# Kernel tuning notes

Measured on AMD Instinct MI355X. Metric: run time of the kernel, lower is better.

Reference implementation:

```python
import jax, jax.numpy as jnp
import numpy as np

B, C, D, H, W = 4, 128, 16, 16, 16
HID = 128
EPS = 1e-5


def setup_inputs() -> dict:
    key = jax.random.key(0)
    ks = jax.random.split(key, 10)
    s = 1.0 / np.sqrt(C)
    return {
        "x": jax.random.normal(ks[0], (B, C, D, H, W), dtype=jnp.float32),
        "Wq": jax.random.normal(ks[1], (HID, C), dtype=jnp.float32) * s,
        "bq": jax.random.normal(ks[2], (HID,), dtype=jnp.float32) * s,
        "Wk": jax.random.normal(ks[3], (HID, C), dtype=jnp.float32) * s,
        "bk": jax.random.normal(ks[4], (HID,), dtype=jnp.float32) * s,
        "Wv": jax.random.normal(ks[5], (HID, C), dtype=jnp.float32) * s,
        "bv": jax.random.normal(ks[6], (HID,), dtype=jnp.float32) * s,
        "bn_weight": jax.random.normal(ks[7], (HID,), dtype=jnp.float32),
        "bn_bias": jax.random.normal(ks[8], (HID,), dtype=jnp.float32),
        "gamma": jax.random.normal(ks[9], (1,), dtype=jnp.float32),
    }


def reference(x, Wq, bq, Wk, bk, Wv, bv, bn_weight, bn_bias, gamma):
    b, c, d, h, w = x.shape
    n = d * h * w
    xf = x.reshape(b, c, n)  # [B, C, N]
    # 1x1 conv3d == per-voxel linear: [B, hid, N]
    q = jnp.einsum("hc,bcn->bnh", Wq, xf) + bq  # [B, N, hid] (query permuted)
    k = jnp.einsum("hc,bcn->bhn", Wk, xf) + bk[None, :, None]  # [B, hid, N]
    v = jnp.einsum("hc,bcn->bhn", Wv, xf) + bv[None, :, None]  # [B, hid, N]
    # unscaled attention scores [B, N, N], softmax over last dim
    attn = jax.nn.softmax(jnp.einsum("bih,bhj->bij", q, k), axis=-1)
    # out[b,h,i] = sum_j v[b,h,j] * attn[b,i,j]
    out = jnp.einsum("bhj,bij->bhi", v, attn)  # [B, hid, N]
    # BatchNorm3d (training mode): per-channel stats over (B, N), biased var
    mean = jnp.mean(out, axis=(0, 2), keepdims=True)
    var = jnp.mean(jnp.square(out - mean), axis=(0, 2), keepdims=True)
    out = (out - mean) * jax.lax.rsqrt(var + EPS)
    out = out * bn_weight[None, :, None] + bn_bias[None, :, None]
    out = gamma[0] * out.reshape(b, c, d, h, w) + x
    return out
```

## Files before the change

kernel.cpp:

```cpp
#include <hip/hip_runtime.h>


#define NV 4096
#define LOG2E 1.44269504088896340736f
#define EPSV 1e-5f

typedef float f32x4 __attribute__((ext_vector_type(4)));
typedef short bf16x8 __attribute__((ext_vector_type(8)));
typedef unsigned short u16x4 __attribute__((ext_vector_type(4)));
typedef unsigned int u32x2 __attribute__((ext_vector_type(2)));

static __device__ __forceinline__ unsigned short f2bf(float f) {
    union { float f; unsigned u; } v; v.f = f;
    unsigned r = v.u + 0x7FFFu + ((v.u >> 16) & 1u);
    return (unsigned short)(r >> 16);
}
static __device__ __forceinline__ float bf2f(unsigned short u) {
    union { unsigned u; float f; } v; v.u = ((unsigned)u) << 16; return v.f;
}
static __device__ __forceinline__ unsigned fbits(float f) {
    union { float f; unsigned u; } v; v.f = f; return v.u;
}

__global__ __launch_bounds__(256) void convw_kernel(
    const float* __restrict__ Wq, const float* __restrict__ Wk,
    const float* __restrict__ Wv, unsigned short* __restrict__ Wbf)
{
    int i = blockIdx.x * 256 + threadIdx.x;
    const float* src = (i < 16384) ? Wq : (i < 32768 ? Wk : Wv);
    Wbf[i] = f2bf(src[i & 16383]);
}

__global__ __launch_bounds__(256) void xt_kernel(
    const float* __restrict__ x, unsigned short* __restrict__ xT)
{
    __shared__ unsigned short st[64 * 132];
    const int b = blockIdx.x >> 6, n0 = (blockIdx.x & 63) << 6;
    const int t = threadIdx.x;
    #pragma unroll
    for (int it = 0; it < 32; ++it) {
        const int e = it * 256 + t;
        const int c = e >> 6, il = e & 63;
        st[il * 132 + c] = f2bf(x[(((b << 7) + c) << 12) + n0 + il]);
    }
    __syncthreads();
    unsigned short* dst = xT + (((b << 12) + n0) << 7);
    #pragma unroll
    for (int it = 0; it < 32; ++it) {
        const int e = it * 256 + t;
        const int il = e >> 7, c = e & 127;
        dst[(il << 7) + c] = st[il * 132 + c];
    }
}

__global__ __launch_bounds__(256) void proj_kernel(
    const unsigned short* __restrict__ xT,
    const unsigned short* __restrict__ Wbf,
    const float* __restrict__ bq, const float* __restrict__ bk,
    const float* __restrict__ bv,
    unsigned short* __restrict__ Qb, unsigned short* __restrict__ Kb,
    unsigned short* __restrict__ Vb)
{
    __shared__ unsigned short vtile[128 * 66];
    const int bid = blockIdx.x;
    const int m = bid >> 8, b = (bid >> 6) & 3, n0 = (bid & 63) << 6;
    const int t = threadIdx.x, w = t >> 6, lane = t & 63;
    const int quad = lane >> 4, l16 = lane & 15;
    const int vb = n0 + (w << 4);

    bf16x8 af[4];
    {
        const unsigned short* xr = xT + (((b << 12) + vb + l16) << 7) + (quad << 3);
        #pragma unroll
        for (int ck = 0; ck < 4; ++ck) af[ck] = *(const bf16x8*)(xr + (ck << 5));
    }
    const unsigned short* Wm = Wbf + (m << 14);
    const float* bias = (m == 0) ? bq : ((m == 1) ? bk : bv);
    unsigned short* dst = (m == 0) ? Qb : Kb;

    #pragma unroll
    for (int s = 0; s < 8; ++s) {
        const int h = (s << 4) + l16;
        f32x4 acc = {0.f, 0.f, 0.f, 0.f};
        #pragma unroll
        for (int ck = 0; ck < 4; ++ck) {
            bf16x8 wf = *(const bf16x8*)(Wm + (h << 7) + (ck << 5) + (quad << 3));
            acc = __builtin_amdgcn_mfma_f32_16x16x32_bf16(af[ck], wf, acc, 0, 0, 0);
        }
        const float bval = bias[h];
        if (m == 2) {
            #pragma unroll
            for (int r = 0; r < 4; ++r)
                vtile[h * 66 + (w << 4) + (quad << 2) + r] = f2bf(acc[r] + bval);
        } else {
            #pragma unroll
            for (int r = 0; r < 4; ++r) {
                const int n = vb + (quad << 2) + r;
                dst[(((b << 12) + n) << 7) + h] = f2bf(acc[r] + bval);
            }
        }
    }
    if (m == 2) {
        __syncthreads();
        #pragma unroll
        for (int it = 0; it < 32; ++it) {
            const int e = it * 256 + t;
            const int h = e >> 6, il = e & 63;
            Vb[(((b << 7) + h) << 12) + n0 + il] = vtile[h * 66 + il];
        }
    }
}

template<int NSL>
__global__ __launch_bounds__(256, 2) void flash_kernel(
    const unsigned short* __restrict__ Qb,
    const unsigned short* __restrict__ Kb,
    const unsigned short* __restrict__ Vb,
    unsigned short* __restrict__ Opart, float* __restrict__ lpart,
    unsigned short* __restrict__ Obuf)
{
    __shared__ unsigned short Kt[64 * 128];
    __shared__ unsigned short Vt[128 * 64];
    __shared__ unsigned short pA[4][32 * 72];
    const int bid = blockIdx.x;
    const int sl = bid >> 7, b = (bid >> 5) & 3, ic = bid & 31;
    const int t = threadIdx.x, w = t >> 6, lane = t & 63;
    const int quad = lane >> 4, l16 = lane & 15;
    const int iw = (ic << 7) + (w << 5);
    const int jbase = sl * (NV / NSL);
    unsigned short* pAw = pA[w];

    const int ktg = t & 15, ktj = t >> 4;
    const int vtg = t & 7,  vth = t >> 3;
    const int kswz = (ktg ^ ktj) << 3;
    const int vswz = (vtg ^ (vth & 7)) << 3;

    bf16x8 qf[2][4];
    #pragma unroll
    for (int half = 0; half < 2; ++half) {
        const unsigned short* qp =
            Qb + (((b << 12) + iw + (half << 4) + l16) << 7) + (quad << 3);
        #pragma unroll
        for (int ck = 0; ck < 4; ++ck) qf[half][ck] = *(const bf16x8*)(qp + (ck << 5));
    }
    f32x4 Oacc[2][8];
    #pragma unroll
    for (int half = 0; half < 2; ++half)
        #pragma unroll
        for (int s = 0; s < 8; ++s) Oacc[half][s] = (f32x4){0.f, 0.f, 0.f, 0.f};
    float lsum0 = 0.f, lsum1 = 0.f;

    const unsigned short* Kbb = Kb + ((long)b << 19);
    const unsigned short* Vbb = Vb + ((long)b << 19);

    for (int t8 = 0; t8 < (NV / NSL) >> 6; ++t8) {
        const int j0 = jbase + (t8 << 6);

        __syncthreads();
        bf16x8 sk[4], sv[4];
        #pragma unroll
        for (int r = 0; r < 4; ++r)
            sk[r] = *(const bf16x8*)(Kbb + ((j0 + (r << 4) + ktj) << 7) + (ktg << 3));
        #pragma unroll
        for (int r = 0; r < 4; ++r)
            sv[r] = *(const bf16x8*)(Vbb + (((r << 5) + vth) << 12) + j0 + (vtg << 3));
        #pragma unroll
        for (int r = 0; r < 4; ++r)
            *(bf16x8*)(Kt + (((r << 4) + ktj) << 7) + kswz) = sk[r];
        #pragma unroll
        for (int r = 0; r < 4; ++r)
            *(bf16x8*)(Vt + (((r << 5) + vth) << 6) + vswz) = sv[r];
        __syncthreads();

        #pragma unroll
        for (int js = 0; js < 4; ++js) {
            bf16x8 kf[4];
            const int krow = ((js << 4) + l16) << 7;
            #pragma unroll
            for (int ck = 0; ck < 4; ++ck)
                kf[ck] = *(const bf16x8*)(Kt + krow + ((((ck << 2) + quad) ^ l16) << 3));
            f32x4 a0 = {0.f, 0.f, 0.f, 0.f}, a1 = {0.f, 0.f, 0.f, 0.f};
            #pragma unroll
            for (int ck = 0; ck < 4; ++ck) {
                a0 = __builtin_amdgcn_mfma_f32_16x16x32_bf16(kf[ck], qf[0][ck], a0, 0, 0, 0);
                a1 = __builtin_amdgcn_mfma_f32_16x16x32_bf16(kf[ck], qf[1][ck], a1, 0, 0, 0);
            }
            f32x4 e0, e1;
            #pragma unroll
            for (int r = 0; r < 4; ++r) {
                e0[r] = exp2f(a0[r] * LOG2E);
                e1[r] = exp2f(a1[r] * LOG2E);
            }
            lsum0 += (e0[0] + e0[1]) + (e0[2] + e0[3]);
            lsum1 += (e1[0] + e1[1]) + (e1[2] + e1[3]);
            u32x2 pk0, pk1;
            pk0[0] = __builtin_amdgcn_perm(fbits(e0[1]), fbits(e0[0]), 0x07060302u);
            pk0[1] = __builtin_amdgcn_perm(fbits(e0[3]), fbits(e0[2]), 0x07060302u);
            pk1[0] = __builtin_amdgcn_perm(fbits(e1[1]), fbits(e1[0]), 0x07060302u);
            pk1[1] = __builtin_amdgcn_perm(fbits(e1[3]), fbits(e1[2]), 0x07060302u);
            const int jc = (js << 4) + (quad << 2);
            *(u32x2*)(pAw + l16 * 72 + jc)        = pk0;
            *(u32x2*)(pAw + (16 + l16) * 72 + jc) = pk1;
        }
        bf16x8 pf[2][2];
        #pragma unroll
        for (int half = 0; half < 2; ++half)
            #pragma unroll
            for (int kh = 0; kh < 2; ++kh)
                pf[half][kh] = *(const bf16x8*)(pAw + ((half << 4) + l16) * 72 +
                                                (kh << 5) + (quad << 3));
        #pragma unroll
        for (int s = 0; s < 8; ++s) {
            const int vrow = ((s << 4) + l16) << 6;
            const bf16x8 v0 = *(const bf16x8*)(Vt + vrow + ((quad ^ (l16 & 7)) << 3));
            const bf16x8 v1 = *(const bf16x8*)(Vt + vrow + (((4 + quad) ^ (l16 & 7)) << 3));
            Oacc[0][s] = __builtin_amdgcn_mfma_f32_16x16x32_bf16(v0, pf[0][0], Oacc[0][s], 0, 0, 0);
            Oacc[0][s] = __builtin_amdgcn_mfma_f32_16x16x32_bf16(v1, pf[0][1], Oacc[0][s], 0, 0, 0);
            Oacc[1][s] = __builtin_amdgcn_mfma_f32_16x16x32_bf16(v0, pf[1][0], Oacc[1][s], 0, 0, 0);
            Oacc[1][s] = __builtin_amdgcn_mfma_f32_16x16x32_bf16(v1, pf[1][1], Oacc[1][s], 0, 0, 0);
        }
    }

    float l0 = lsum0; l0 += __shfl_xor(l0, 16); l0 += __shfl_xor(l0, 32);
    float l1 = lsum1; l1 += __shfl_xor(l1, 16); l1 += __shfl_xor(l1, 32);

    if (NSL == 1) {
        const float rl0 = 1.f / l0, rl1 = 1.f / l1;
        #pragma unroll
        for (int s = 0; s < 8; ++s)
            #pragma unroll
            for (int r = 0; r < 4; ++r) {
                const int h = (s << 4) + (quad << 2) + r;
                Obuf[(((b << 7) + h) << 12) + iw + l16]      = f2bf(Oacc[0][s][r] * rl0);
                Obuf[(((b << 7) + h) << 12) + iw + 16 + l16] = f2bf(Oacc[1][s][r] * rl1);
            }
    } else {
        const int slb = (sl << 2) + b;
        if (quad == 0) {
            lpart[(slb << 12) + iw + l16]      = l0;
            lpart[(slb << 12) + iw + 16 + l16] = l1;
        }
        unsigned short* Ob = Opart + ((long)slb << 19);
        #pragma unroll
        for (int half = 0; half < 2; ++half)
            #pragma unroll
            for (int s = 0; s < 8; ++s)
                #pragma unroll
                for (int r = 0; r < 4; ++r) {
                    const int h = (s << 4) + (quad << 2) + r;
                    Ob[(h << 12) + iw + (half << 4) + l16] = f2bf(Oacc[half][s][r]);
                }
    }
}

template<int NSL>
__global__ __launch_bounds__(256) void merge_kernel(
    const unsigned short* __restrict__ Opart, const float* __restrict__ lpart,
    unsigned short* __restrict__ Obuf, float* __restrict__ psums)
{
    const int bid = blockIdx.x;
    const int b = bid >> 9, h = (bid >> 2) & 127, iq = bid & 3;
    const int t = threadIdx.x;
    const int ibase = (iq << 10) + (t << 2);
    float a0 = 0.f, a1 = 0.f, a2 = 0.f, a3 = 0.f;
    float t0 = 0.f, t1 = 0.f, t2 = 0.f, t3 = 0.f;
    #pragma unroll
    for (int sl = 0; sl < NSL; ++sl) {
        const int slb = (sl << 2) + b;
        const u16x4 u  = *(const u16x4*)(Opart + ((long)slb << 19) + ((long)h << 12) + ibase);
        const float4 lv = *(const float4*)(lpart + (slb << 12) + ibase);
        a0 += bf2f(u[0]); a1 += bf2f(u[1]); a2 += bf2f(u[2]); a3 += bf2f(u[3]);
        t0 += lv.x; t1 += lv.y; t2 += lv.z; t3 += lv.w;
    }
    const float o0 = a0 / t0, o1 = a1 / t1, o2 = a2 / t2, o3 = a3 / t3;
    u16x4 o;
    o[0] = f2bf(o0); o[1] = f2bf(o1); o[2] = f2bf(o2); o[3] = f2bf(o3);
    *(u16x4*)(Obuf + (((b << 7) + h) << 12) + ibase) = o;

    float so  = o0 + o1 + o2 + o3;
    float so2 = o0*o0 + o1*o1 + o2*o2 + o3*o3;
    #pragma unroll
    for (int off = 32; off; off >>= 1) {
        so  += __shfl_down(so, off);
        so2 += __shfl_down(so2, off);
    }
    __shared__ float rb[8];
    const int wv = t >> 6;
    if ((t & 63) == 0) { rb[wv] = so; rb[4 + wv] = so2; }
    __syncthreads();
    if (t == 0) {
        psums[bid]        = rb[0] + rb[1] + rb[2] + rb[3];
        psums[2048 + bid] = rb[4] + rb[5] + rb[6] + rb[7];
    }
}

__global__ __launch_bounds__(256) void bnsum_kernel(
    const unsigned short* __restrict__ Obuf, float* __restrict__ psums)
{
    const int bid = blockIdx.x;
    const int b = bid >> 9, h = (bid >> 2) & 127, iq = bid & 3;
    const int t = threadIdx.x;
    const int ibase = (iq << 10) + (t << 2);
    const u16x4 u = *(const u16x4*)(Obuf + (((b << 7) + h) << 12) + ibase);
    const float x0 = bf2f(u[0]), x1 = bf2f(u[1]), x2 = bf2f(u[2]), x3 = bf2f(u[3]);
    float so  = x0 + x1 + x2 + x3;
    float so2 = x0*x0 + x1*x1 + x2*x2 + x3*x3;
    #pragma unroll
    for (int off = 32; off; off >>= 1) {
        so  += __shfl_down(so, off);
        so2 += __shfl_down(so2, off);
    }
    __shared__ float rb[8];
    const int wv = t >> 6;
    if ((t & 63) == 0) { rb[wv] = so; rb[4 + wv] = so2; }
    __syncthreads();
    if (t == 0) {
        psums[bid]        = rb[0] + rb[1] + rb[2] + rb[3];
        psums[2048 + bid] = rb[4] + rb[5] + rb[6] + rb[7];
    }
}

__global__ __launch_bounds__(256) void final_kernel(
    const unsigned short* __restrict__ Obuf, const float* __restrict__ x,
    const float* __restrict__ psums, const float* __restrict__ bnw,
    const float* __restrict__ bnb, const float* __restrict__ gammap,
    float* __restrict__ out)
{
    const int bid = blockIdx.x;
    const int c = (bid >> 2) & 127;
    const int t = threadIdx.x;
    const int li = t & 15;
    const int pid = ((li >> 2) << 9) + (c << 2) + (li & 3);
    float s  = psums[pid];
    float ss = psums[2048 + pid];
    s += __shfl_xor(s, 1, 16); ss += __shfl_xor(ss, 1, 16);
    s += __shfl_xor(s, 2, 16); ss += __shfl_xor(ss, 2, 16);
    s += __shfl_xor(s, 4, 16); ss += __shfl_xor(ss, 4, 16);
    s += __shfl_xor(s, 8, 16); ss += __shfl_xor(ss, 8, 16);
    const float inv = 1.f / 16384.f;
    const float mean = s * inv;
    const float var  = ss * inv - mean * mean;
    const float g = gammap[0];
    const float scale = bnw[c] * rsqrtf(var + EPSV);
    const float a  = g * scale;
    const float bb = g * (bnb[c] - mean * scale);

    const int base = (bid * 256 + t) << 2;
    const u16x4 u = *(const u16x4*)(Obuf + base);
    const float4 xv = *(const float4*)(x + base);
    float4 r;
    r.x = bf2f(u[0]) * a + bb + xv.x;
    r.y = bf2f(u[1]) * a + bb + xv.y;
    r.z = bf2f(u[2]) * a + bb + xv.z;
    r.w = bf2f(u[3]) * a + bb + xv.w;
    *(float4*)(out + base) = r;
}

extern "C" void kernel_launch(void* const* d_in, const int* in_sizes, int n_in,
                              void* d_out, int out_size, void* d_ws, size_t ws_size,
                              hipStream_t stream) {
    const float* x   = (const float*)d_in[0];
    const float* Wq  = (const float*)d_in[1];
    const float* bq  = (const float*)d_in[2];
    const float* Wk  = (const float*)d_in[3];
    const float* bk  = (const float*)d_in[4];
    const float* Wv  = (const float*)d_in[5];
    const float* bv  = (const float*)d_in[6];
    const float* bnw = (const float*)d_in[7];
    const float* bnb = (const float*)d_in[8];
    const float* gam = (const float*)d_in[9];
    float* out = (float*)d_out;

    char* ws = (char*)d_ws;
    unsigned short* xT   = (unsigned short*)(ws);
    unsigned short* Obuf = (unsigned short*)(ws);
    unsigned short* Qb   = (unsigned short*)(ws + (4u  << 20));
    unsigned short* Kb   = (unsigned short*)(ws + (8u  << 20));
    unsigned short* Vb   = (unsigned short*)(ws + (12u << 20));
    unsigned short* Wbf  = (unsigned short*)(ws + (16u << 20));
    float*          lpart = (float*)(ws + (16u << 20) + (128u << 10));
    float*          psums = (float*)(ws + (16u << 20) + (640u << 10));
    unsigned short* Opart = (unsigned short*)(ws + (17u << 20));

    int nsl = 1;
    if      (ws_size >= (17ull << 20) + (32ull << 20)) nsl = 8;
    else if (ws_size >= (17ull << 20) + (16ull << 20)) nsl = 4;
    else if (ws_size >= (17ull << 20) + (8ull  << 20)) nsl = 2;

    convw_kernel<<<192, 256, 0, stream>>>(Wq, Wk, Wv, Wbf);
    xt_kernel<<<256, 256, 0, stream>>>(x, xT);
    proj_kernel<<<768, 256, 0, stream>>>(xT, Wbf, bq, bk, bv, Qb, Kb, Vb);
    if (nsl == 8) {
        flash_kernel<8><<<1024, 256, 0, stream>>>(Qb, Kb, Vb, Opart, lpart, Obuf);
        merge_kernel<8><<<2048, 256, 0, stream>>>(Opart, lpart, Obuf, psums);
    } else if (nsl == 4) {
        flash_kernel<4><<<512, 256, 0, stream>>>(Qb, Kb, Vb, Opart, lpart, Obuf);
        merge_kernel<4><<<2048, 256, 0, stream>>>(Opart, lpart, Obuf, psums);
    } else if (nsl == 2) {
        flash_kernel<2><<<256, 256, 0, stream>>>(Qb, Kb, Vb, Opart, lpart, Obuf);
        merge_kernel<2><<<2048, 256, 0, stream>>>(Opart, lpart, Obuf, psums);
    } else {
        flash_kernel<1><<<128, 256, 0, stream>>>(Qb, Kb, Vb, Opart, lpart, Obuf);
        bnsum_kernel<<<2048, 256, 0, stream>>>(Obuf, psums);
    }
    final_kernel<<<2048, 256, 0, stream>>>(Obuf, x, psums, bnw, bnb, gam, out);
}
```

Measured before the change: 160.2 us.

## Fuse projection prep kernels and merge split-softmax with batchnorm finalize

```diff
diff --git a/kernel.cpp b/kernel.cpp
--- a/kernel.cpp
+++ b/kernel.cpp
@@ -8,6 +8,7 @@
 typedef float f32x4 __attribute__((ext_vector_type(4)));
 typedef short bf16x8 __attribute__((ext_vector_type(8)));
 typedef unsigned short u16x4 __attribute__((ext_vector_type(4)));
+typedef unsigned short u16x8 __attribute__((ext_vector_type(8)));
 typedef unsigned int u32x2 __attribute__((ext_vector_type(2)));
 
 static __device__ __forceinline__ unsigned short f2bf(float f) {
@@ -22,92 +23,86 @@
     union { float f; unsigned u; } v; v.f = f; return v.u;
 }
 
-__global__ __launch_bounds__(256) void convw_kernel(
+__global__ __launch_bounds__(256) void projx_kernel(
+    const float* __restrict__ x,
     const float* __restrict__ Wq, const float* __restrict__ Wk,
-    const float* __restrict__ Wv, unsigned short* __restrict__ Wbf)
-{
-    int i = blockIdx.x * 256 + threadIdx.x;
-    const float* src = (i < 16384) ? Wq : (i < 32768 ? Wk : Wv);
-    Wbf[i] = f2bf(src[i & 16383]);
-}
-
-__global__ __launch_bounds__(256) void xt_kernel(
-    const float* __restrict__ x, unsigned short* __restrict__ xT)
-{
-    __shared__ unsigned short st[64 * 132];
-    const int b = blockIdx.x >> 6, n0 = (blockIdx.x & 63) << 6;
-    const int t = threadIdx.x;
-    #pragma unroll
-    for (int it = 0; it < 32; ++it) {
-        const int e = it * 256 + t;
-        const int c = e >> 6, il = e & 63;
-        st[il * 132 + c] = f2bf(x[(((b << 7) + c) << 12) + n0 + il]);
-    }
-    __syncthreads();
-    unsigned short* dst = xT + (((b << 12) + n0) << 7);
-    #pragma unroll
-    for (int it = 0; it < 32; ++it) {
-        const int e = it * 256 + t;
-        const int il = e >> 7, c = e & 127;
-        dst[(il << 7) + c] = st[il * 132 + c];
-    }
-}
-
-__global__ __launch_bounds__(256) void proj_kernel(
-    const unsigned short* __restrict__ xT,
-    const unsigned short* __restrict__ Wbf,
+    const float* __restrict__ Wv,
     const float* __restrict__ bq, const float* __restrict__ bk,
     const float* __restrict__ bv,
     unsigned short* __restrict__ Qb, unsigned short* __restrict__ Kb,
     unsigned short* __restrict__ Vb)
 {
+    __shared__ unsigned short xt[64 * 136];
+    __shared__ unsigned short Wl[128 * 136];
     __shared__ unsigned short vtile[128 * 66];
-    const int bid = blockIdx.x;
-    const int m = bid >> 8, b = (bid >> 6) & 3, n0 = (bid & 63) << 6;
+    const int b = blockIdx.x >> 6, n0 = (blockIdx.x & 63) << 6;
     const int t = threadIdx.x, w = t >> 6, lane = t & 63;
     const int quad = lane >> 4, l16 = lane & 15;
-    const int vb = n0 + (w << 4);
+
+    #pragma unroll
+    for (int it = 0; it < 32; ++it) {
+        const int e = it * 256 + t;
+        const int c = e >> 6, il = e & 63;
+        xt[il * 136 + c] = f2bf(x[(((b << 7) + c) << 12) + n0 + il]);
+    }
+    __syncthreads();
 
     bf16x8 af[4];
     {
-        const unsigned short* xr = xT + (((b << 12) + vb + l16) << 7) + (quad << 3);
-        #pragma unroll
-        for (int ck = 0; ck < 4; ++ck) af[ck] = *(const bf16x8*)(xr + (ck << 5));
-    }
-    const unsigned short* Wm = Wbf + (m << 14);
-    const float* bias = (m == 0) ? bq : ((m == 1) ? bk : bv);
-    unsigned short* dst = (m == 0) ? Qb : Kb;
-
-    #pragma unroll
-    for (int s = 0; s < 8; ++s) {
-        const int h = (s << 4) + l16;
-        f32x4 acc = {0.f, 0.f, 0.f, 0.f};
-        #pragma unroll
-        for (int ck = 0; ck < 4; ++ck) {
-            bf16x8 wf = *(const bf16x8*)(Wm + (h << 7) + (ck << 5) + (quad << 3));
-            acc = __builtin_amdgcn_mfma_f32_16x16x32_bf16(af[ck], wf, acc, 0, 0, 0);
-        }
-        const float bval = bias[h];
-        if (m == 2) {
-            #pragma unroll
-            for (int r = 0; r < 4; ++r)
-                vtile[h * 66 + (w << 4) + (quad << 2) + r] = f2bf(acc[r] + bval);
-        } else {
-            #pragma unroll
-            for (int r = 0; r < 4; ++r) {
-                const int n = vb + (quad << 2) + r;
-                dst[(((b << 12) + n) << 7) + h] = f2bf(acc[r] + bval);
+        const int il = (w << 4) + l16;
+        #pragma unroll
+        for (int ck = 0; ck < 4; ++ck)
+            af[ck] = *(const bf16x8*)(xt + il * 136 + (ck << 5) + (quad << 3));
+    }
+    const int vb = n0 + (w << 4);
+    const float* Ws[3] = {Wq, Wk, Wv};
+    const float* bs[3] = {bq, bk, bv};
+
+    for (int m = 0; m < 3; ++m) {
+        __syncthreads();
+        #pragma unroll
+        for (int it = 0; it < 16; ++it) {
+            const int idx = it * 1024 + (t << 2);
+            const float4 wv4 = *(const float4*)(Ws[m] + idx);
+            const int h = idx >> 7, c = idx & 127;
+            u16x4 pk;
+            pk[0] = f2bf(wv4.x); pk[1] = f2bf(wv4.y);
+            pk[2] = f2bf(wv4.z); pk[3] = f2bf(wv4.w);
+            *(u16x4*)(Wl + h * 136 + c) = pk;
+        }
+        __syncthreads();
+
+        const float* bias = bs[m];
+        unsigned short* dst = (m == 0) ? Qb : Kb;
+        #pragma unroll
+        for (int s = 0; s < 8; ++s) {
+            const int h = (s << 4) + l16;
+            f32x4 acc = {0.f, 0.f, 0.f, 0.f};
+            #pragma unroll
+            for (int ck = 0; ck < 4; ++ck) {
+                const bf16x8 wf = *(const bf16x8*)(Wl + h * 136 + (ck << 5) + (quad << 3));
+                acc = __builtin_amdgcn_mfma_f32_16x16x32_bf16(af[ck], wf, acc, 0, 0, 0);
             }
-        }
-    }
-    if (m == 2) {
-        __syncthreads();
-        #pragma unroll
-        for (int it = 0; it < 32; ++it) {
-            const int e = it * 256 + t;
-            const int h = e >> 6, il = e & 63;
-            Vb[(((b << 7) + h) << 12) + n0 + il] = vtile[h * 66 + il];
-        }
+            const float bval = bias[h];
+            if (m == 2) {
+                #pragma unroll
+                for (int r = 0; r < 4; ++r)
+                    vtile[h * 66 + (w << 4) + (quad << 2) + r] = f2bf(acc[r] + bval);
+            } else {
+                #pragma unroll
+                for (int r = 0; r < 4; ++r) {
+                    const int n = vb + (quad << 2) + r;
+                    dst[(((b << 12) + n) << 7) + h] = f2bf(acc[r] + bval);
+                }
+            }
+        }
+    }
+    __syncthreads();
+    #pragma unroll
+    for (int it = 0; it < 32; ++it) {
+        const int e = it * 256 + t;
+        const int h = e >> 6, il = e & 63;
+        Vb[(((b << 7) + h) << 12) + n0 + il] = vtile[h * 66 + il];
     }
 }
 
@@ -155,7 +150,6 @@
 
     for (int t8 = 0; t8 < (NV / NSL) >> 6; ++t8) {
         const int j0 = jbase + (t8 << 6);
-
         __syncthreads();
         bf16x8 sk[4], sv[4];
         #pragma unroll
@@ -254,106 +248,131 @@
 }
 
 template<int NSL>
-__global__ __launch_bounds__(256) void merge_kernel(
+__global__ __launch_bounds__(1024) void mf_kernel(
     const unsigned short* __restrict__ Opart, const float* __restrict__ lpart,
-    unsigned short* __restrict__ Obuf, float* __restrict__ psums)
-{
-    const int bid = blockIdx.x;
-    const int b = bid >> 9, h = (bid >> 2) & 127, iq = bid & 3;
-    const int t = threadIdx.x;
-    const int ibase = (iq << 10) + (t << 2);
-    float a0 = 0.f, a1 = 0.f, a2 = 0.f, a3 = 0.f;
-    float t0 = 0.f, t1 = 0.f, t2 = 0.f, t3 = 0.f;
-    #pragma unroll
-    for (int sl = 0; sl < NSL; ++sl) {
-        const int slb = (sl << 2) + b;
-        const u16x4 u  = *(const u16x4*)(Opart + ((long)slb << 19) + ((long)h << 12) + ibase);
-        const float4 lv = *(const float4*)(lpart + (slb << 12) + ibase);
-        a0 += bf2f(u[0]); a1 += bf2f(u[1]); a2 += bf2f(u[2]); a3 += bf2f(u[3]);
-        t0 += lv.x; t1 += lv.y; t2 += lv.z; t3 += lv.w;
-    }
-    const float o0 = a0 / t0, o1 = a1 / t1, o2 = a2 / t2, o3 = a3 / t3;
-    u16x4 o;
-    o[0] = f2bf(o0); o[1] = f2bf(o1); o[2] = f2bf(o2); o[3] = f2bf(o3);
-    *(u16x4*)(Obuf + (((b << 7) + h) << 12) + ibase) = o;
-
-    float so  = o0 + o1 + o2 + o3;
-    float so2 = o0*o0 + o1*o1 + o2*o2 + o3*o3;
-    #pragma unroll
-    for (int off = 32; off; off >>= 1) {
-        so  += __shfl_down(so, off);
-        so2 += __shfl_down(so2, off);
-    }
-    __shared__ float rb[8];
-    const int wv = t >> 6;
-    if ((t & 63) == 0) { rb[wv] = so; rb[4 + wv] = so2; }
-    __syncthreads();
-    if (t == 0) {
-        psums[bid]        = rb[0] + rb[1] + rb[2] + rb[3];
-        psums[2048 + bid] = rb[4] + rb[5] + rb[6] + rb[7];
-    }
-}
-
-__global__ __launch_bounds__(256) void bnsum_kernel(
-    const unsigned short* __restrict__ Obuf, float* __restrict__ psums)
-{
-    const int bid = blockIdx.x;
-    const int b = bid >> 9, h = (bid >> 2) & 127, iq = bid & 3;
-    const int t = threadIdx.x;
-    const int ibase = (iq << 10) + (t << 2);
-    const u16x4 u = *(const u16x4*)(Obuf + (((b << 7) + h) << 12) + ibase);
-    const float x0 = bf2f(u[0]), x1 = bf2f(u[1]), x2 = bf2f(u[2]), x3 = bf2f(u[3]);
-    float so  = x0 + x1 + x2 + x3;
-    float so2 = x0*x0 + x1*x1 + x2*x2 + x3*x3;
-    #pragma unroll
-    for (int off = 32; off; off >>= 1) {
-        so  += __shfl_down(so, off);
-        so2 += __shfl_down(so2, off);
-    }
-    __shared__ float rb[8];
-    const int wv = t >> 6;
-    if ((t & 63) == 0) { rb[wv] = so; rb[4 + wv] = so2; }
-    __syncthreads();
-    if (t == 0) {
-        psums[bid]        = rb[0] + rb[1] + rb[2] + rb[3];
-        psums[2048 + bid] = rb[4] + rb[5] + rb[6] + rb[7];
-    }
-}
-
-__global__ __launch_bounds__(256) void final_kernel(
-    const unsigned short* __restrict__ Obuf, const float* __restrict__ x,
-    const float* __restrict__ psums, const float* __restrict__ bnw,
+    const float* __restrict__ x, const float* __restrict__ bnw,
     const float* __restrict__ bnb, const float* __restrict__ gammap,
     float* __restrict__ out)
 {
-    const int bid = blockIdx.x;
-    const int c = (bid >> 2) & 127;
+    const int h = blockIdx.x;
     const int t = threadIdx.x;
-    const int li = t & 15;
-    const int pid = ((li >> 2) << 9) + (c << 2) + (li & 3);
-    float s  = psums[pid];
-    float ss = psums[2048 + pid];
-    s += __shfl_xor(s, 1, 16); ss += __shfl_xor(ss, 1, 16);
-    s += __shfl_xor(s, 2, 16); ss += __shfl_xor(ss, 2, 16);
-    s += __shfl_xor(s, 4, 16); ss += __shfl_xor(ss, 4, 16);
-    s += __shfl_xor(s, 8, 16); ss += __shfl_xor(ss, 8, 16);
+    const int b = t >> 8;
+    const int i0 = (t & 255) << 4;
+
+    float A[16], L[16];
+    #pragma unroll
+    for (int k = 0; k < 16; ++k) { A[k] = 0.f; L[k] = 0.f; }
+    #pragma unroll
+    for (int sl = 0; sl < NSL; ++sl) {
+        const int slb = (sl << 2) + b;
+        const u16x8 u0 = *(const u16x8*)(Opart + ((long)slb << 19) + ((long)h << 12) + i0);
+        const u16x8 u1 = *(const u16x8*)(Opart + ((long)slb << 19) + ((long)h << 12) + i0 + 8);
+        const float* lp = lpart + (slb << 12) + i0;
+        #pragma unroll
+        for (int k = 0; k < 8; ++k) { A[k] += bf2f(u0[k]); A[8 + k] += bf2f(u1[k]); }
+        #pragma unroll
+        for (int k = 0; k < 4; ++k) {
+            const float4 lv = *(const float4*)(lp + (k << 2));
+            L[(k << 2) + 0] += lv.x; L[(k << 2) + 1] += lv.y;
+            L[(k << 2) + 2] += lv.z; L[(k << 2) + 3] += lv.w;
+        }
+    }
+    float o[16], s = 0.f, ss = 0.f;
+    #pragma unroll
+    for (int k = 0; k < 16; ++k) {
+        o[k] = A[k] / L[k];
+        s += o[k]; ss += o[k] * o[k];
+    }
+    #pragma unroll
+    for (int off = 32; off; off >>= 1) {
+        s  += __shfl_down(s, off);
+        ss += __shfl_down(ss, off);
+    }
+    __shared__ float rs[16], rss[16], fin[2];
+    const int wid = t >> 6;
+    if ((t & 63) == 0) { rs[wid] = s; rss[wid] = ss; }
+    __syncthreads();
+    if (t == 0) {
+        float s2 = 0.f, ss2 = 0.f;
+        #pragma unroll
+        for (int k = 0; k < 16; ++k) { s2 += rs[k]; ss2 += rss[k]; }
+        fin[0] = s2; fin[1] = ss2;
+    }
+    __syncthreads();
     const float inv = 1.f / 16384.f;
-    const float mean = s * inv;
-    const float var  = ss * inv - mean * mean;
+    const float mean = fin[0] * inv;
+    const float var  = fin[1] * inv - mean * mean;
     const float g = gammap[0];
-    const float scale = bnw[c] * rsqrtf(var + EPSV);
+    const float scale = bnw[h] * rsqrtf(var + EPSV);
     const float a  = g * scale;
-    const float bb = g * (bnb[c] - mean * scale);
-
-    const int base = (bid * 256 + t) << 2;
-    const u16x4 u = *(const u16x4*)(Obuf + base);
-    const float4 xv = *(const float4*)(x + base);
-    float4 r;
-    r.x = bf2f(u[0]) * a + bb + xv.x;
-    r.y = bf2f(u[1]) * a + bb + xv.y;
-    r.z = bf2f(u[2]) * a + bb + xv.z;
-    r.w = bf2f(u[3]) * a + bb + xv.w;
-    *(float4*)(out + base) = r;
+    const float bb = g * (bnb[h] - mean * scale);
+
+    const float* xp = x + (((b << 7) + h) << 12) + i0;
+    float* op = out + (((b << 7) + h) << 12) + i0;
+    #pragma unroll
+    for (int k = 0; k < 4; ++k) {
+        const float4 xv = *(const float4*)(xp + (k << 2));
+        float4 r;
+        r.x = o[(k << 2) + 0] * a + bb + xv.x;
+        r.y = o[(k << 2) + 1] * a + bb + xv.y;
+        r.z = o[(k << 2) + 2] * a + bb + xv.z;
+        r.w = o[(k << 2) + 3] * a + bb + xv.w;
+        *(float4*)(op + (k << 2)) = r;
+    }
+}
+
+__global__ __launch_bounds__(1024) void mf1_kernel(
+    const unsigned short* __restrict__ Obuf,
+    const float* __restrict__ x, const float* __restrict__ bnw,
+    const float* __restrict__ bnb, const float* __restrict__ gammap,
+    float* __restrict__ out)
+{
+    const int h = blockIdx.x;
+    const int t = threadIdx.x;
+    const int b = t >> 8;
+    const int i0 = (t & 255) << 4;
+    const u16x8 u0 = *(const u16x8*)(Obuf + (((b << 7) + h) << 12) + i0);
+    const u16x8 u1 = *(const u16x8*)(Obuf + (((b << 7) + h) << 12) + i0 + 8);
+    float o[16], s = 0.f, ss = 0.f;
+    #pragma unroll
+    for (int k = 0; k < 8; ++k) { o[k] = bf2f(u0[k]); o[8 + k] = bf2f(u1[k]); }
+    #pragma unroll
+    for (int k = 0; k < 16; ++k) { s += o[k]; ss += o[k] * o[k]; }
+    #pragma unroll
+    for (int off = 32; off; off >>= 1) {
+        s  += __shfl_down(s, off);
+        ss += __shfl_down(ss, off);
+    }
+    __shared__ float rs[16], rss[16], fin[2];
+    const int wid = t >> 6;
+    if ((t & 63) == 0) { rs[wid] = s; rss[wid] = ss; }
+    __syncthreads();
+    if (t == 0) {
+        float s2 = 0.f, ss2 = 0.f;
+        #pragma unroll
+        for (int k = 0; k < 16; ++k) { s2 += rs[k]; ss2 += rss[k]; }
+        fin[0] = s2; fin[1] = ss2;
+    }
+    __syncthreads();
+    const float inv = 1.f / 16384.f;
+    const float mean = fin[0] * inv;
+    const float var  = fin[1] * inv - mean * mean;
+    const float g = gammap[0];
+    const float scale = bnw[h] * rsqrtf(var + EPSV);
+    const float a  = g * scale;
+    const float bb = g * (bnb[h] - mean * scale);
+    const float* xp = x + (((b << 7) + h) << 12) + i0;
+    float* op = out + (((b << 7) + h) << 12) + i0;
+    #pragma unroll
+    for (int k = 0; k < 4; ++k) {
+        const float4 xv = *(const float4*)(xp + (k << 2));
+        float4 r;
+        r.x = o[(k << 2) + 0] * a + bb + xv.x;
+        r.y = o[(k << 2) + 1] * a + bb + xv.y;
+        r.z = o[(k << 2) + 2] * a + bb + xv.z;
+        r.w = o[(k << 2) + 3] * a + bb + xv.w;
+        *(float4*)(op + (k << 2)) = r;
+    }
 }
 
 extern "C" void kernel_launch(void* const* d_in, const int* in_sizes, int n_in,
@@ -372,14 +391,11 @@
     float* out = (float*)d_out;
 
     char* ws = (char*)d_ws;
-    unsigned short* xT   = (unsigned short*)(ws);
     unsigned short* Obuf = (unsigned short*)(ws);
     unsigned short* Qb   = (unsigned short*)(ws + (4u  << 20));
     unsigned short* Kb   = (unsigned short*)(ws + (8u  << 20));
     unsigned short* Vb   = (unsigned short*)(ws + (12u << 20));
-    unsigned short* Wbf  = (unsigned short*)(ws + (16u << 20));
     float*          lpart = (float*)(ws + (16u << 20) + (128u << 10));
-    float*          psums = (float*)(ws + (16u << 20) + (640u << 10));
     unsigned short* Opart = (unsigned short*)(ws + (17u << 20));
 
     int nsl = 1;
@@ -387,21 +403,18 @@
     else if (ws_size >= (17ull << 20) + (16ull << 20)) nsl = 4;
     else if (ws_size >= (17ull << 20) + (8ull  << 20)) nsl = 2;
 
-    convw_kernel<<<192, 256, 0, stream>>>(Wq, Wk, Wv, Wbf);
-    xt_kernel<<<256, 256, 0, stream>>>(x, xT);
-    proj_kernel<<<768, 256, 0, stream>>>(xT, Wbf, bq, bk, bv, Qb, Kb, Vb);
+    projx_kernel<<<256, 256, 0, stream>>>(x, Wq, Wk, Wv, bq, bk, bv, Qb, Kb, Vb);
     if (nsl == 8) {
         flash_kernel<8><<<1024, 256, 0, stream>>>(Qb, Kb, Vb, Opart, lpart, Obuf);
-        merge_kernel<8><<<2048, 256, 0, stream>>>(Opart, lpart, Obuf, psums);
+        mf_kernel<8><<<128, 1024, 0, stream>>>(Opart, lpart, x, bnw, bnb, gam, out);
     } else if (nsl == 4) {
         flash_kernel<4><<<512, 256, 0, stream>>>(Qb, Kb, Vb, Opart, lpart, Obuf);
-        merge_kernel<4><<<2048, 256, 0, stream>>>(Opart, lpart, Obuf, psums);
+        mf_kernel<4><<<128, 1024, 0, stream>>>(Opart, lpart, x, bnw, bnb, gam, out);
     } else if (nsl == 2) {
         flash_kernel<2><<<256, 256, 0, stream>>>(Qb, Kb, Vb, Opart, lpart, Obuf);
-        merge_kernel<2><<<2048, 256, 0, stream>>>(Opart, lpart, Obuf, psums);
+        mf_kernel<2><<<128, 1024, 0, stream>>>(Opart, lpart, x, bnw, bnb, gam, out);
     } else {
         flash_kernel<1><<<128, 256, 0, stream>>>(Qb, Kb, Vb, Opart, lpart, Obuf);
-        bnsum_kernel<<<2048, 256, 0, stream>>>(Obuf, psums);
-    }
-    final_kernel<<<2048, 256, 0, stream>>>(Obuf, x, psums, bnw, bnb, gam, out);
-}
+        mf1_kernel<<<128, 1024, 0, stream>>>(Obuf, x, bnw, bnb, gam, out);
+    }
+}
```

Result: slower. 166.4 us (+3.9%).
